# Kernel tuning notes

Measured on AMD Instinct MI355X. Metric: run time of the kernel, lower is better.

The kernel has to match this reference:

```python
import jax, jax.numpy as jnp
import numpy as np

N, L, E, H = 2, 2048, 1024, 16
DH = E // H  # head_dim = 64


def setup_inputs() -> dict:
    key = jax.random.key(0)
    ks = jax.random.split(key, 11)
    s_h = 1.0 / np.sqrt(DH)
    s_e = 1.0 / np.sqrt(E)
    return {
        "EP_q": jax.random.normal(ks[0], (N, L, E), jnp.float32),
        "EP_k": jax.random.normal(ks[1], (N, L, E), jnp.float32),
        "EP_v": jax.random.normal(ks[2], (N, L, E), jnp.float32),
        "W_q": jax.random.uniform(ks[3], (DH, DH), jnp.float32, -s_h, s_h),
        "b_q": jax.random.uniform(ks[4], (DH,), jnp.float32, -s_h, s_h),
        "W_k": jax.random.uniform(ks[5], (DH, DH), jnp.float32, -s_h, s_h),
        "b_k": jax.random.uniform(ks[6], (DH,), jnp.float32, -s_h, s_h),
        "W_v": jax.random.uniform(ks[7], (DH, DH), jnp.float32, -s_h, s_h),
        "b_v": jax.random.uniform(ks[8], (DH,), jnp.float32, -s_h, s_h),
        "W_o": jax.random.uniform(ks[9], (E, E), jnp.float32, -s_e, s_e),
        "b_o": jax.random.uniform(ks[10], (E,), jnp.float32, -s_e, s_e),
    }


def reference(EP_q, EP_k, EP_v, W_q, b_q, W_k, b_k, W_v, b_v, W_o, b_o):
    n, q_len = EP_q.shape[0], EP_q.shape[1]
    # split into heads: (N, L, H, DH)
    q = EP_q.reshape(n, q_len, H, DH)
    k = EP_k.reshape(n, EP_k.shape[1], H, DH)
    v = EP_v.reshape(n, EP_v.shape[1], H, DH)
    # per-head linear (same weights across heads), torch Linear: x @ W.T + b
    Q = q @ W_q.T + b_q
    K = k @ W_k.T + b_k
    V = v @ W_v.T + b_v
    # scores (N, H, Lq, Lk); NOTE: scaled by sqrt(embed_size) per original code
    scores = jnp.einsum("nqhd,nkhd->nhqk", Q, K) / jnp.sqrt(jnp.float32(E))
    attn = jax.nn.softmax(scores, axis=-1)
    out = jnp.einsum("nhqk,nkhd->nqhd", attn, V).reshape(n, q_len, E)
    return out @ W_o.T + b_o
```

## Files before the change

kernel.cpp:

```cpp
#include <hip/hip_runtime.h>

#define N_B 2
#define L_L 2048
#define E_E 1024
#define H_H 16
#define D_H 64
#define LDSP 72

typedef __bf16 bf16x8 __attribute__((ext_vector_type(8)));
typedef float f32x4 __attribute__((ext_vector_type(4)));
typedef short s16x8 __attribute__((ext_vector_type(8)));
typedef unsigned short u16x4 __attribute__((ext_vector_type(4)));

__device__ __forceinline__ f32x4 mfma16(bf16x8 a, bf16x8 b, f32x4 c) {
  return __builtin_amdgcn_mfma_f32_16x16x32_bf16(a, b, c, 0, 0, 0);
}

__device__ __forceinline__ unsigned short f2bf(float x) {
  unsigned int u = __float_as_uint(x);
  u = (u + 0x7fffu + ((u >> 16) & 1u)) >> 16;
  return (unsigned short)u;
}

__device__ __forceinline__ unsigned int cvtpk(float lo, float hi) {
  unsigned int r;
  asm("v_cvt_pk_bf16_f32 %0, %1, %2" : "=v"(r) : "v"(lo), "v"(hi));
  return r;
}

__device__ __forceinline__ void swap32(unsigned int& a, unsigned int& b) {
  asm("v_permlane32_swap_b32 %0, %1" : "+v"(a), "+v"(b));
}
__device__ __forceinline__ void swap16(unsigned int& a, unsigned int& b) {
  asm("v_permlane16_swap_b32 %0, %1" : "+v"(a), "+v"(b));
}

__device__ __forceinline__ float max3f(float a, float b, float c) {
  float r;
  asm("v_max3_f32 %0, %1, %2, %3" : "=v"(r) : "v"(a), "v"(b), "v"(c));
  return r;
}

__device__ __forceinline__ float exp2a(float x) {
  float r;
  asm("v_exp_f32 %0, %1" : "=v"(r) : "v"(x));
  return r;
}

__device__ __forceinline__ void gload16(const void* g, void* l) {
  __builtin_amdgcn_global_load_lds(
      (__attribute__((address_space(1))) void*)g,
      (__attribute__((address_space(3))) void*)l, 16, 0, 0);
}

__device__ __forceinline__ bf16x8 pack_frag(float p0, float p1, float p2, float p3,
                                            float p4, float p5, float p6, float p7) {
  unsigned int x0 = cvtpk(p0, p1), x1 = cvtpk(p2, p3);
  unsigned int x2 = cvtpk(p4, p5), x3 = cvtpk(p6, p7);
  swap32(x0, x2); swap16(x0, x2);
  swap32(x1, x3); swap16(x1, x3);
  union { unsigned int u[4]; bf16x8 v; } f;
  f.u[0] = x0; f.u[1] = x1; f.u[2] = x2; f.u[3] = x3;
  return f.v;
}

__global__ __launch_bounds__(256) void qkv_gemm_kernel(
    const float* __restrict__ EPq, const float* __restrict__ EPk, const float* __restrict__ EPv,
    const float* __restrict__ Wq, const float* __restrict__ Wk, const float* __restrict__ Wv,
    const float* __restrict__ bq, const float* __restrict__ bk, const float* __restrict__ bv,
    const float* __restrict__ Wo, unsigned short* __restrict__ Wob,
    unsigned short* __restrict__ Qb, unsigned short* __restrict__ Kb,
    unsigned short* __restrict__ Vtb) {
  __shared__ __attribute__((aligned(16))) unsigned short Xs[64][LDSP];
  __shared__ __attribute__((aligned(16))) unsigned short Ws[64][LDSP];
  const int tid = threadIdx.x;
  const int wid = tid >> 6;
  const int lane = tid & 63;
  const int lr = lane & 15;
  const int lg = lane >> 4;
  const int nh = blockIdx.x >> 5;
  const int l0 = (blockIdx.x & 31) * 64;
  const int n = nh >> 4;
  const int h = nh & 15;
  const float SCQ = 0.03125f * 1.44269504089f;

  {
    const int i = blockIdx.x * 256 + tid;
    const float4 f = ((const float4*)Wo)[i];
    u16x4 v = { f2bf(f.x), f2bf(f.y), f2bf(f.z), f2bf(f.w) };
    *(u16x4*)&Wob[(size_t)i * 4] = v;
  }

  #pragma unroll
  for (int mat = 0; mat < 3; ++mat) {
    const float* X = (mat == 0) ? EPq : (mat == 1) ? EPk : EPv;
    const float* W = (mat == 0) ? Wq : (mat == 1) ? Wk : Wv;
    const float* bias = (mat == 0) ? bq : (mat == 1) ? bk : bv;
    const float osc = (mat == 0) ? SCQ : 1.0f;

    const float* xb = X + ((size_t)(n * L_L + l0)) * E_E + h * D_H;
    #pragma unroll
    for (int it = 0; it < 4; ++it) {
      const int idx = it * 256 + tid;
      const int row = idx >> 4, c = idx & 15;
      const float4 f = *(const float4*)(xb + (size_t)row * E_E + c * 4);
      u16x4 v = { f2bf(f.x), f2bf(f.y), f2bf(f.z), f2bf(f.w) };
      *(u16x4*)&Xs[row][c * 4] = v;
    }
    #pragma unroll
    for (int it = 0; it < 4; ++it) {
      const int idx = it * 256 + tid;
      const int row = idx >> 4, c = idx & 15;
      const float4 f = *(const float4*)(W + idx * 4);
      u16x4 v = { f2bf(f.x), f2bf(f.y), f2bf(f.z), f2bf(f.w) };
      *(u16x4*)&Ws[row][c * 4] = v;
    }
    __syncthreads();

    const bf16x8 a0 = *(const bf16x8*)&Xs[wid * 16 + lr][lg * 8];
    const bf16x8 a1 = *(const bf16x8*)&Xs[wid * 16 + lr][32 + lg * 8];
    f32x4 acc[4];
    #pragma unroll
    for (int t = 0; t < 4; ++t) {
      const float bb = bias[t * 16 + lr];
      acc[t] = f32x4{bb, bb, bb, bb};
      const bf16x8 b0 = *(const bf16x8*)&Ws[t * 16 + lr][lg * 8];
      const bf16x8 b1 = *(const bf16x8*)&Ws[t * 16 + lr][32 + lg * 8];
      acc[t] = mfma16(a0, b0, acc[t]);
      acc[t] = mfma16(a1, b1, acc[t]);
    }
    __syncthreads();

    #pragma unroll
    for (int t = 0; t < 4; ++t)
      #pragma unroll
      for (int r = 0; r < 4; ++r)
        Xs[wid * 16 + lg * 4 + r][t * 16 + lr] = f2bf(acc[t][r] * osc);
    __syncthreads();

    if (mat < 2) {
      unsigned short* dst = ((mat == 0) ? Qb : Kb) + ((size_t)nh * L_L + l0) * D_H;
      #pragma unroll
      for (int it = 0; it < 2; ++it) {
        const int idx = it * 256 + tid;
        const int row = idx >> 3, c = idx & 7;
        *(s16x8*)(dst + (size_t)row * D_H + c * 8) = *(s16x8*)&Xs[row][c * 8];
      }
    } else {
      #pragma unroll
      for (int it = 0; it < 2; ++it) {
        const int idx = it * 256 + tid;
        const int d = idx & 63, c = idx >> 6;
        s16x8 v;
        #pragma unroll
        for (int j = 0; j < 8; ++j) v[j] = (short)Xs[c * 8 + j][d];
        *(s16x8*)(Vtb + ((size_t)nh * D_H + d) * L_L + l0 + c * 8) = v;
      }
    }
    __syncthreads();
  }
}

__global__ __launch_bounds__(512, 4) void attn_mfma_kernel(
    const unsigned short* __restrict__ Qb, const unsigned short* __restrict__ Kb,
    const unsigned short* __restrict__ Vtb, unsigned short* __restrict__ Ab) {
  __shared__ __attribute__((aligned(16))) unsigned short KS[2][2][64][64];
  __shared__ __attribute__((aligned(16))) unsigned short VS[2][2][64][64];

  const int tid = threadIdx.x;
  const int wid = tid >> 6;
  const int wq = wid & 3;
  const int kw = wid >> 2;
  const int lane = tid & 63;
  const int lr = lane & 15;
  const int lg = lane >> 4;

  const int bid = ((blockIdx.x & 7) << 6) + (blockIdx.x >> 3);
  const int nh = bid >> 4;
  const int q0w = ((bid & 15) << 7) + wq * 32;

  const unsigned short* gQ = Qb + ((size_t)nh * L_L + q0w) * D_H;

  bf16x8 bQ[2][2];
  #pragma unroll
  for (int qb = 0; qb < 2; ++qb)
    #pragma unroll
    for (int c2 = 0; c2 < 2; ++c2)
      bQ[qb][c2] = *(const bf16x8*)(gQ + (qb * 16 + lr) * D_H + c2 * 32 + lg * 8);

  const s16x8 ones16 = {0x3F80,0x3F80,0x3F80,0x3F80,0x3F80,0x3F80,0x3F80,0x3F80};
  const bf16x8 ones = *(const bf16x8*)&ones16;

  const int sh = tid >> 8;
  const int tid8 = tid & 255;
  const int srow0 = tid8 >> 3, sch0 = tid8 & 7;
  const int srow1 = srow0 + 32;
  const int kc0 = (sch0 ^ (srow0 & 7)) * 8;
  const int kc1 = (sch0 ^ (srow1 & 7)) * 8;
  const unsigned short* gKs = Kb + ((size_t)nh * L_L + sh * 1024) * D_H;
  const unsigned short* gVs = Vtb + (size_t)nh * D_H * L_L + sh * 1024;

  #define STAGE(buf, ktoff)                                                    \
    do {                                                                       \
      unsigned short* kd = &KS[sh][buf][0][0];                                 \
      unsigned short* vd = &VS[sh][buf][0][0];                                 \
      gload16(gKs + (size_t)((ktoff) * 64 + srow0) * D_H + kc0,                \
              kd + srow0 * 64 + sch0 * 8);                                     \
      gload16(gKs + (size_t)((ktoff) * 64 + srow1) * D_H + kc1,                \
              kd + srow1 * 64 + sch0 * 8);                                     \
      gload16(gVs + (size_t)srow0 * L_L + (ktoff) * 64 + kc0,                  \
              vd + srow0 * 64 + sch0 * 8);                                     \
      gload16(gVs + (size_t)srow1 * L_L + (ktoff) * 64 + kc1,                  \
              vd + srow1 * 64 + sch0 * 8);                                     \
    } while (0)

  STAGE(0, 0);
  __syncthreads();

  f32x4 acc0[4] = {f32x4{0,0,0,0},f32x4{0,0,0,0},f32x4{0,0,0,0},f32x4{0,0,0,0}};
  f32x4 acc1[4] = {f32x4{0,0,0,0},f32x4{0,0,0,0},f32x4{0,0,0,0},f32x4{0,0,0,0}};
  f32x4 lacc0 = {0,0,0,0}, lacc1 = {0,0,0,0};
  float m0 = -1e30f, m1 = -1e30f;
  int cur = 0;

  for (int kt = 0; kt < 16; ++kt) {
    STAGE(cur ^ 1, ((kt + 1) & 15));

    const char* Kcur = (const char*)&KS[kw][cur][0][0];
    const char* Vcur = (const char*)&VS[kw][cur][0][0];

    float sv0[16], sv1[16];
    __builtin_amdgcn_s_setprio(1);
    #pragma unroll
    for (int kb = 0; kb < 4; ++kb) {
      const int row = kb * 16 + lr;
      const bf16x8 a0 = *(const bf16x8*)(Kcur + row * 128 + ((lg ^ (row & 7)) << 4));
      const bf16x8 a1 = *(const bf16x8*)(Kcur + row * 128 + (((4 + lg) ^ (row & 7)) << 4));
      f32x4 c0 = {0,0,0,0}, c1 = {0,0,0,0};
      c0 = mfma16(a0, bQ[0][0], c0); c0 = mfma16(a1, bQ[0][1], c0);
      c1 = mfma16(a0, bQ[1][0], c1); c1 = mfma16(a1, bQ[1][1], c1);
      #pragma unroll
      for (int r = 0; r < 4; ++r) { sv0[kb*4+r] = c0[r]; sv1[kb*4+r] = c1[r]; }
    }
    __builtin_amdgcn_s_setprio(0);

    float mt0 = max3f(sv0[0], sv0[1], sv0[2]);
    float mt1 = max3f(sv1[0], sv1[1], sv1[2]);
    #pragma unroll
    for (int j = 3; j < 15; j += 2) {
      mt0 = max3f(mt0, sv0[j], sv0[j+1]);
      mt1 = max3f(mt1, sv1[j], sv1[j+1]);
    }
    mt0 = fmaxf(mt0, sv0[15]);
    mt1 = fmaxf(mt1, sv1[15]);

    const bool defer = (mt0 - m0 <= 8.0f) && (mt1 - m1 <= 8.0f);
    if (!__all(defer)) {
      float v0 = fmaxf(mt0, __shfl_xor(mt0, 16)); v0 = fmaxf(v0, __shfl_xor(v0, 32));
      float v1 = fmaxf(mt1, __shfl_xor(mt1, 16)); v1 = fmaxf(v1, __shfl_xor(v1, 32));
      const float mn0 = fmaxf(m0, v0), mn1 = fmaxf(m1, v1);
      const float sc0f = exp2a(m0 - mn0), sc1f = exp2a(m1 - mn1);
      m0 = mn0; m1 = mn1;
      #pragma unroll
      for (int r = 0; r < 4; ++r) {
        const float sa0 = __shfl(sc0f, 4 * lg + r);
        const float sa1 = __shfl(sc1f, 4 * lg + r);
        #pragma unroll
        for (int t = 0; t < 4; ++t) { acc0[t][r] *= sa0; acc1[t][r] *= sa1; }
        lacc0[r] *= sa0; lacc1[r] *= sa1;
      }
    }

    #pragma unroll
    for (int j = 0; j < 16; ++j) {
      sv0[j] = exp2a(sv0[j] - m0);
      sv1[j] = exp2a(sv1[j] - m1);
    }

    bf16x8 aP0[2], aP1[2];
    aP0[0] = pack_frag(sv0[0], sv0[1], sv0[2], sv0[3], sv0[4], sv0[5], sv0[6], sv0[7]);
    aP0[1] = pack_frag(sv0[8], sv0[9], sv0[10], sv0[11], sv0[12], sv0[13], sv0[14], sv0[15]);
    aP1[0] = pack_frag(sv1[0], sv1[1], sv1[2], sv1[3], sv1[4], sv1[5], sv1[6], sv1[7]);
    aP1[1] = pack_frag(sv1[8], sv1[9], sv1[10], sv1[11], sv1[12], sv1[13], sv1[14], sv1[15]);

    __builtin_amdgcn_s_setprio(1);
    lacc0 = mfma16(aP0[0], ones, lacc0); lacc0 = mfma16(aP0[1], ones, lacc0);
    lacc1 = mfma16(aP1[0], ones, lacc1); lacc1 = mfma16(aP1[1], ones, lacc1);
    #pragma unroll
    for (int t = 0; t < 4; ++t) {
      const int row = t * 16 + lr;
      const bf16x8 v0 = *(const bf16x8*)(Vcur + row * 128 + ((lg ^ (row & 7)) << 4));
      const bf16x8 v1 = *(const bf16x8*)(Vcur + row * 128 + (((4 + lg) ^ (row & 7)) << 4));
      acc0[t] = mfma16(aP0[0], v0, acc0[t]); acc0[t] = mfma16(aP0[1], v1, acc0[t]);
      acc1[t] = mfma16(aP1[0], v0, acc1[t]); acc1[t] = mfma16(aP1[1], v1, acc1[t]);
    }
    __builtin_amdgcn_s_setprio(0);

    __syncthreads();
    cur ^= 1;
  }
  #undef STAGE

  float mq0[4], mq1[4];
  #pragma unroll
  for (int r = 0; r < 4; ++r) {
    mq0[r] = __shfl(m0, 4 * lg + r);
    mq1[r] = __shfl(m1, 4 * lg + r);
  }
  float* accL = (float*)&KS[0][0][0][0];
  float* mlL  = (float*)&VS[0][0][0][0];
  if (kw == 1) {
    const int base = wq * 2048 + lane * 4;
    #pragma unroll
    for (int t = 0; t < 4; ++t) {
      *(f32x4*)&accL[base + t * 256] = acc0[t];
      *(f32x4*)&accL[base + 1024 + t * 256] = acc1[t];
    }
    if (lr == 0) {
      #pragma unroll
      for (int r = 0; r < 4; ++r) {
        const int q = 4 * lg + r;
        *(float2*)&mlL[wq * 128 + q * 2]      = float2{mq0[r], lacc0[r]};
        *(float2*)&mlL[wq * 128 + 64 + q * 2] = float2{mq1[r], lacc1[r]};
      }
    }
  }
  __syncthreads();
  if (kw == 0) {
    const int n = nh >> 4, h = nh & 15;
    const int base = wq * 2048 + lane * 4;
    #pragma unroll
    for (int qb = 0; qb < 2; ++qb) {
      const f32x4* accA = qb ? acc1 : acc0;
      const f32x4 lA4 = qb ? lacc1 : lacc0;
      const float* mqA = qb ? mq1 : mq0;
      #pragma unroll
      for (int r = 0; r < 4; ++r) {
        const int q = 4 * lg + r;
        const float2 mlB = *(const float2*)&mlL[wq * 128 + qb * 64 + q * 2];
        const float M = fmaxf(mqA[r], mlB.x);
        const float wA = exp2a(mqA[r] - M), wB = exp2a(mlB.x - M);
        const float invL = 1.0f / (lA4[r] * wA + mlB.y * wB);
        #pragma unroll
        for (int t = 0; t < 4; ++t) {
          const float ob = accL[base + qb * 1024 + t * 256 + r];
          const float o = (accA[t][r] * wA + ob * wB) * invL;
          Ab[((size_t)(n * L_L + q0w + qb * 16 + q)) * E_E + h * D_H + t * 16 + lr] =
              f2bf(o);
        }
      }
    }
  }
}

__global__ __launch_bounds__(256, 2) void out_gemm_kernel(
    const unsigned short* __restrict__ Ab, const unsigned short* __restrict__ Wob,
    const float* __restrict__ bo, float* __restrict__ out) {
  __shared__ __attribute__((aligned(16))) unsigned short As[2][64][64];
  __shared__ __attribute__((aligned(16))) unsigned short Bs[2][128][64];
  const int tid = threadIdx.x;
  const int wid = tid >> 6;
  const int lane = tid & 63;
  const int lr = lane & 15;
  const int lg = lane >> 4;

  const int bid = ((blockIdx.x & 7) << 6) + (blockIdx.x >> 3);
  const int m0 = (bid >> 3) * 64;
  const int n0 = (bid & 7) * 128;
  const int wr = wid >> 1, wc = wid & 1;

  const int r0 = tid >> 3, sc = tid & 7;
  const int scol = (sc ^ (r0 & 7)) * 8;

  #define OSTAGE(buf, kt)                                                      \
    do {                                                                       \
      unsigned short* ad = &As[buf][0][0];                                     \
      unsigned short* bd = &Bs[buf][0][0];                                     \
      gload16(Ab + (size_t)(m0 + r0) * E_E + (kt) * 64 + scol,                 \
              ad + r0 * 64 + sc * 8);                                          \
      gload16(Ab + (size_t)(m0 + r0 + 32) * E_E + (kt) * 64 + scol,            \
              ad + (r0 + 32) * 64 + sc * 8);                                   \
      gload16(Wob + (size_t)(n0 + r0) * E_E + (kt) * 64 + scol,                \
              bd + r0 * 64 + sc * 8);                                          \
      gload16(Wob + (size_t)(n0 + r0 + 32) * E_E + (kt) * 64 + scol,           \
              bd + (r0 + 32) * 64 + sc * 8);                                   \
      gload16(Wob + (size_t)(n0 + r0 + 64) * E_E + (kt) * 64 + scol,           \
              bd + (r0 + 64) * 64 + sc * 8);                                   \
      gload16(Wob + (size_t)(n0 + r0 + 96) * E_E + (kt) * 64 + scol,           \
              bd + (r0 + 96) * 64 + sc * 8);                                   \
    } while (0)

  f32x4 acc[2][4];
  #pragma unroll
  for (int mi = 0; mi < 2; ++mi)
    #pragma unroll
    for (int ni = 0; ni < 4; ++ni) {
      const float bb = bo[n0 + wc * 64 + ni * 16 + lr];
      acc[mi][ni] = f32x4{bb, bb, bb, bb};
    }

  OSTAGE(0, 0);
  __syncthreads();
  int cur = 0;

  for (int kt = 0; kt < 16; ++kt) {
    if (kt < 15) OSTAGE(cur ^ 1, kt + 1);

    const char* Ac = (const char*)&As[cur][0][0];
    const char* Bc = (const char*)&Bs[cur][0][0];
    bf16x8 af[2][2], bfr[4][2];
    #pragma unroll
    for (int mi = 0; mi < 2; ++mi) {
      const int row = wr * 32 + mi * 16 + lr;
      #pragma unroll
      for (int kb = 0; kb < 2; ++kb)
        af[mi][kb] = *(const bf16x8*)(Ac + row * 128 + (((kb * 4 + lg) ^ (row & 7)) << 4));
    }
    #pragma unroll
    for (int ni = 0; ni < 4; ++ni) {
      const int row = wc * 64 + ni * 16 + lr;
      #pragma unroll
      for (int kb = 0; kb < 2; ++kb)
        bfr[ni][kb] = *(const bf16x8*)(Bc + row * 128 + (((kb * 4 + lg) ^ (row & 7)) << 4));
    }
    __builtin_amdgcn_s_setprio(1);
    #pragma unroll
    for (int kb = 0; kb < 2; ++kb)
      #pragma unroll
      for (int mi = 0; mi < 2; ++mi)
        #pragma unroll
        for (int ni = 0; ni < 4; ++ni)
          acc[mi][ni] = mfma16(af[mi][kb], bfr[ni][kb], acc[mi][ni]);
    __builtin_amdgcn_s_setprio(0);

    __syncthreads();
    cur ^= 1;
  }
  #undef OSTAGE

  #pragma unroll
  for (int mi = 0; mi < 2; ++mi)
    #pragma unroll
    for (int ni = 0; ni < 4; ++ni) {
      const int nn = n0 + wc * 64 + ni * 16 + lr;
      #pragma unroll
      for (int r = 0; r < 4; ++r) {
        const int mm = m0 + wr * 32 + mi * 16 + lg * 4 + r;
        out[(size_t)mm * E_E + nn] = acc[mi][ni][r];
      }
    }
}

extern "C" void kernel_launch(void* const* d_in, const int* in_sizes, int n_in,
                              void* d_out, int out_size, void* d_ws, size_t ws_size,
                              hipStream_t stream) {
  const float* EPq = (const float*)d_in[0];
  const float* EPk = (const float*)d_in[1];
  const float* EPv = (const float*)d_in[2];
  const float* Wq  = (const float*)d_in[3];
  const float* bq  = (const float*)d_in[4];
  const float* Wk  = (const float*)d_in[5];
  const float* bk  = (const float*)d_in[6];
  const float* Wv  = (const float*)d_in[7];
  const float* bv  = (const float*)d_in[8];
  const float* Wo  = (const float*)d_in[9];
  const float* bo  = (const float*)d_in[10];
  float* out = (float*)d_out;

  unsigned short* ws = (unsigned short*)d_ws;
  const size_t SZ = (size_t)N_B * H_H * L_L * D_H;
  unsigned short* Qb  = ws;
  unsigned short* Kb  = Qb + SZ;
  unsigned short* Vtb = Kb + SZ;
  unsigned short* Ab  = Vtb + SZ;
  unsigned short* Wob = Ab + SZ;

  qkv_gemm_kernel<<<1024, 256, 0, stream>>>(
      EPq, EPk, EPv, Wq, Wk, Wv, bq, bk, bv, Wo, Wob, Qb, Kb, Vtb);
  attn_mfma_kernel<<<512, 512, 0, stream>>>(Qb, Kb, Vtb, Ab);
  out_gemm_kernel<<<512, 256, 0, stream>>>(Ab, Wob, bo, out);
}
```

Baseline: 79.69 us.

## Software-pipeline QK^T one tile ahead of softmax/PV with triple-buffered K

Restructures the attention main loop so the QK^T MFMAs for the next key tile are issued before the softmax and PV step of the current tile. K gets a three-slot LDS ring and V stays double-buffered, and the loop is unrolled by two with alternating score register sets. The aim is to overlap exp/max VALU work with matrix-core work and hide LDS latency. The cost is more LDS (one extra K slot) and roughly double the score registers, which may reduce occupancy under the 512x4 launch bound.

After: 219.4 us. +175.3%, slower.

```diff
diff --git a/kernel.cpp b/kernel.cpp
--- a/kernel.cpp
+++ b/kernel.cpp
@@ -164,7 +164,7 @@
 __global__ __launch_bounds__(512, 4) void attn_mfma_kernel(
     const unsigned short* __restrict__ Qb, const unsigned short* __restrict__ Kb,
     const unsigned short* __restrict__ Vtb, unsigned short* __restrict__ Ab) {
-  __shared__ __attribute__((aligned(16))) unsigned short KS[2][2][64][64];
+  __shared__ __attribute__((aligned(16))) unsigned short KS[3][2][64][64];
   __shared__ __attribute__((aligned(16))) unsigned short VS[2][2][64][64];
 
   const int tid = threadIdx.x;
@@ -200,106 +200,129 @@
   const unsigned short* gKs = Kb + ((size_t)nh * L_L + sh * 1024) * D_H;
   const unsigned short* gVs = Vtb + (size_t)nh * D_H * L_L + sh * 1024;
 
-  #define STAGE(buf, ktoff)                                                    \
+  #define STAGE_K(slot, ktt)                                                   \
     do {                                                                       \
-      unsigned short* kd = &KS[sh][buf][0][0];                                 \
-      unsigned short* vd = &VS[sh][buf][0][0];                                 \
-      gload16(gKs + (size_t)((ktoff) * 64 + srow0) * D_H + kc0,                \
+      unsigned short* kd = &KS[slot][sh][0][0];                                \
+      gload16(gKs + (size_t)((ktt) * 64 + srow0) * D_H + kc0,                  \
               kd + srow0 * 64 + sch0 * 8);                                     \
-      gload16(gKs + (size_t)((ktoff) * 64 + srow1) * D_H + kc1,                \
+      gload16(gKs + (size_t)((ktt) * 64 + srow1) * D_H + kc1,                  \
               kd + srow1 * 64 + sch0 * 8);                                     \
-      gload16(gVs + (size_t)srow0 * L_L + (ktoff) * 64 + kc0,                  \
+    } while (0)
+  #define STAGE_V(vb, ktt)                                                     \
+    do {                                                                       \
+      unsigned short* vd = &VS[vb][sh][0][0];                                  \
+      gload16(gVs + (size_t)srow0 * L_L + (ktt) * 64 + kc0,                    \
               vd + srow0 * 64 + sch0 * 8);                                     \
-      gload16(gVs + (size_t)srow1 * L_L + (ktoff) * 64 + kc1,                  \
+      gload16(gVs + (size_t)srow1 * L_L + (ktt) * 64 + kc1,                    \
               vd + srow1 * 64 + sch0 * 8);                                     \
     } while (0)
-
-  STAGE(0, 0);
-  __syncthreads();
 
   f32x4 acc0[4] = {f32x4{0,0,0,0},f32x4{0,0,0,0},f32x4{0,0,0,0},f32x4{0,0,0,0}};
   f32x4 acc1[4] = {f32x4{0,0,0,0},f32x4{0,0,0,0},f32x4{0,0,0,0},f32x4{0,0,0,0}};
   f32x4 lacc0 = {0,0,0,0}, lacc1 = {0,0,0,0};
   float m0 = -1e30f, m1 = -1e30f;
-  int cur = 0;
-
-  for (int kt = 0; kt < 16; ++kt) {
-    STAGE(cur ^ 1, ((kt + 1) & 15));
-
-    const char* Kcur = (const char*)&KS[kw][cur][0][0];
-    const char* Vcur = (const char*)&VS[kw][cur][0][0];
-
-    float sv0[16], sv1[16];
-    __builtin_amdgcn_s_setprio(1);
-    #pragma unroll
-    for (int kb = 0; kb < 4; ++kb) {
-      const int row = kb * 16 + lr;
-      const bf16x8 a0 = *(const bf16x8*)(Kcur + row * 128 + ((lg ^ (row & 7)) << 4));
-      const bf16x8 a1 = *(const bf16x8*)(Kcur + row * 128 + (((4 + lg) ^ (row & 7)) << 4));
-      f32x4 c0 = {0,0,0,0}, c1 = {0,0,0,0};
-      c0 = mfma16(a0, bQ[0][0], c0); c0 = mfma16(a1, bQ[0][1], c0);
-      c1 = mfma16(a0, bQ[1][0], c1); c1 = mfma16(a1, bQ[1][1], c1);
-      #pragma unroll
-      for (int r = 0; r < 4; ++r) { sv0[kb*4+r] = c0[r]; sv1[kb*4+r] = c1[r]; }
-    }
-    __builtin_amdgcn_s_setprio(0);
-
-    float mt0 = max3f(sv0[0], sv0[1], sv0[2]);
-    float mt1 = max3f(sv1[0], sv1[1], sv1[2]);
-    #pragma unroll
-    for (int j = 3; j < 15; j += 2) {
-      mt0 = max3f(mt0, sv0[j], sv0[j+1]);
-      mt1 = max3f(mt1, sv1[j], sv1[j+1]);
-    }
-    mt0 = fmaxf(mt0, sv0[15]);
-    mt1 = fmaxf(mt1, sv1[15]);
-
-    const bool defer = (mt0 - m0 <= 8.0f) && (mt1 - m1 <= 8.0f);
-    if (!__all(defer)) {
-      float v0 = fmaxf(mt0, __shfl_xor(mt0, 16)); v0 = fmaxf(v0, __shfl_xor(v0, 32));
-      float v1 = fmaxf(mt1, __shfl_xor(mt1, 16)); v1 = fmaxf(v1, __shfl_xor(v1, 32));
-      const float mn0 = fmaxf(m0, v0), mn1 = fmaxf(m1, v1);
-      const float sc0f = exp2a(m0 - mn0), sc1f = exp2a(m1 - mn1);
-      m0 = mn0; m1 = mn1;
-      #pragma unroll
-      for (int r = 0; r < 4; ++r) {
-        const float sa0 = __shfl(sc0f, 4 * lg + r);
-        const float sa1 = __shfl(sc1f, 4 * lg + r);
-        #pragma unroll
-        for (int t = 0; t < 4; ++t) { acc0[t][r] *= sa0; acc1[t][r] *= sa1; }
-        lacc0[r] *= sa0; lacc1[r] *= sa1;
+  float svA0[16], svA1[16], svB0[16], svB1[16];
+
+  #define QKT(SV0, SV1, ks)                                                    \
+    do {                                                                       \
+      const char* Kc = (const char*)&KS[ks][kw][0][0];                         \
+      _Pragma("unroll")                                                        \
+      for (int kb = 0; kb < 4; ++kb) {                                         \
+        const int row = kb * 16 + lr;                                          \
+        const bf16x8 a0 = *(const bf16x8*)(Kc + row * 128 + ((lg ^ (row & 7)) << 4)); \
+        const bf16x8 a1 = *(const bf16x8*)(Kc + row * 128 + (((4 + lg) ^ (row & 7)) << 4)); \
+        f32x4 c0 = {0,0,0,0}, c1 = {0,0,0,0};                                  \
+        c0 = mfma16(a0, bQ[0][0], c0); c0 = mfma16(a1, bQ[0][1], c0);          \
+        c1 = mfma16(a0, bQ[1][0], c1); c1 = mfma16(a1, bQ[1][1], c1);          \
+        _Pragma("unroll")                                                      \
+        for (int r = 0; r < 4; ++r) { SV0[kb*4+r] = c0[r]; SV1[kb*4+r] = c1[r]; } \
+      }                                                                        \
+    } while (0)
+
+  #define SMPV(SV0, SV1, vb)                                                   \
+    do {                                                                       \
+      float mt0 = max3f(SV0[0], SV0[1], SV0[2]);                               \
+      float mt1 = max3f(SV1[0], SV1[1], SV1[2]);                               \
+      _Pragma("unroll")                                                        \
+      for (int j = 3; j < 15; j += 2) {                                        \
+        mt0 = max3f(mt0, SV0[j], SV0[j+1]);                                    \
+        mt1 = max3f(mt1, SV1[j], SV1[j+1]);                                    \
+      }                                                                        \
+      mt0 = fmaxf(mt0, SV0[15]); mt1 = fmaxf(mt1, SV1[15]);                    \
+      const bool defer = (mt0 - m0 <= 8.0f) && (mt1 - m1 <= 8.0f);             \
+      if (!__all(defer)) {                                                     \
+        float v0 = fmaxf(mt0, __shfl_xor(mt0, 16)); v0 = fmaxf(v0, __shfl_xor(v0, 32)); \
+        float v1 = fmaxf(mt1, __shfl_xor(mt1, 16)); v1 = fmaxf(v1, __shfl_xor(v1, 32)); \
+        const float mn0 = fmaxf(m0, v0), mn1 = fmaxf(m1, v1);                  \
+        const float sc0f = exp2a(m0 - mn0), sc1f = exp2a(m1 - mn1);            \
+        m0 = mn0; m1 = mn1;                                                    \
+        _Pragma("unroll")                                                      \
+        for (int r = 0; r < 4; ++r) {                                          \
+          const float sa0 = __shfl(sc0f, 4 * lg + r);                          \
+          const float sa1 = __shfl(sc1f, 4 * lg + r);                          \
+          _Pragma("unroll")                                                    \
+          for (int t = 0; t < 4; ++t) { acc0[t][r] *= sa0; acc1[t][r] *= sa1; }\
+          lacc0[r] *= sa0; lacc1[r] *= sa1;                                    \
+        }                                                                      \
+      }                                                                        \
+      _Pragma("unroll")                                                        \
+      for (int j = 0; j < 16; ++j) {                                           \
+        SV0[j] = exp2a(SV0[j] - m0);                                           \
+        SV1[j] = exp2a(SV1[j] - m1);                                           \
+      }                                                                        \
+      bf16x8 aP0[2], aP1[2];                                                   \
+      aP0[0] = pack_frag(SV0[0], SV0[1], SV0[2], SV0[3], SV0[4], SV0[5], SV0[6], SV0[7]); \
+      aP0[1] = pack_frag(SV0[8], SV0[9], SV0[10], SV0[11], SV0[12], SV0[13], SV0[14], SV0[15]); \
+      aP1[0] = pack_frag(SV1[0], SV1[1], SV1[2], SV1[3], SV1[4], SV1[5], SV1[6], SV1[7]); \
+      aP1[1] = pack_frag(SV1[8], SV1[9], SV1[10], SV1[11], SV1[12], SV1[13], SV1[14], SV1[15]); \
+      const char* Vc = (const char*)&VS[vb][kw][0][0];                         \
+      __builtin_amdgcn_s_setprio(1);                                           \
+      lacc0 = mfma16(aP0[0], ones, lacc0); lacc0 = mfma16(aP0[1], ones, lacc0);\
+      lacc1 = mfma16(aP1[0], ones, lacc1); lacc1 = mfma16(aP1[1], ones, lacc1);\
+      _Pragma("unroll")                                                        \
+      for (int t = 0; t < 4; ++t) {                                            \
+        const int row = t * 16 + lr;                                           \
+        const bf16x8 v0 = *(const bf16x8*)(Vc + row * 128 + ((lg ^ (row & 7)) << 4)); \
+        const bf16x8 v1 = *(const bf16x8*)(Vc + row * 128 + (((4 + lg) ^ (row & 7)) << 4)); \
+        acc0[t] = mfma16(aP0[0], v0, acc0[t]); acc0[t] = mfma16(aP0[1], v1, acc0[t]); \
+        acc1[t] = mfma16(aP1[0], v0, acc1[t]); acc1[t] = mfma16(aP1[1], v1, acc1[t]); \
+      }                                                                        \
+      __builtin_amdgcn_s_setprio(0);                                           \
+    } while (0)
+
+  STAGE_K(0, 0);
+  STAGE_K(1, 1);
+  STAGE_V(0, 0);
+  __syncthreads();
+  QKT(svA0, svA1, 0);
+
+  int ksl_w = 2;
+  int ksl_r = 1;
+
+  for (int t2 = 0; t2 < 8; ++t2) {
+    {
+      const int t = 2 * t2;
+      if (t2 < 7) { STAGE_K(ksl_w, t + 2); ksl_w = (ksl_w == 2) ? 0 : ksl_w + 1; }
+      STAGE_V(1, t + 1);
+      QKT(svB0, svB1, ksl_r); ksl_r = (ksl_r == 2) ? 0 : ksl_r + 1;
+      SMPV(svA0, svA1, 0);
+      __syncthreads();
+    }
+    {
+      const int t = 2 * t2 + 1;
+      if (t2 < 7) {
+        STAGE_K(ksl_w, t + 2); ksl_w = (ksl_w == 2) ? 0 : ksl_w + 1;
+        STAGE_V(0, t + 1);
+        QKT(svA0, svA1, ksl_r); ksl_r = (ksl_r == 2) ? 0 : ksl_r + 1;
       }
-    }
-
-    #pragma unroll
-    for (int j = 0; j < 16; ++j) {
-      sv0[j] = exp2a(sv0[j] - m0);
-      sv1[j] = exp2a(sv1[j] - m1);
-    }
-
-    bf16x8 aP0[2], aP1[2];
-    aP0[0] = pack_frag(sv0[0], sv0[1], sv0[2], sv0[3], sv0[4], sv0[5], sv0[6], sv0[7]);
-    aP0[1] = pack_frag(sv0[8], sv0[9], sv0[10], sv0[11], sv0[12], sv0[13], sv0[14], sv0[15]);
-    aP1[0] = pack_frag(sv1[0], sv1[1], sv1[2], sv1[3], sv1[4], sv1[5], sv1[6], sv1[7]);
-    aP1[1] = pack_frag(sv1[8], sv1[9], sv1[10], sv1[11], sv1[12], sv1[13], sv1[14], sv1[15]);
-
-    __builtin_amdgcn_s_setprio(1);
-    lacc0 = mfma16(aP0[0], ones, lacc0); lacc0 = mfma16(aP0[1], ones, lacc0);
-    lacc1 = mfma16(aP1[0], ones, lacc1); lacc1 = mfma16(aP1[1], ones, lacc1);
-    #pragma unroll
-    for (int t = 0; t < 4; ++t) {
-      const int row = t * 16 + lr;
-      const bf16x8 v0 = *(const bf16x8*)(Vcur + row * 128 + ((lg ^ (row & 7)) << 4));
-      const bf16x8 v1 = *(const bf16x8*)(Vcur + row * 128 + (((4 + lg) ^ (row & 7)) << 4));
-      acc0[t] = mfma16(aP0[0], v0, acc0[t]); acc0[t] = mfma16(aP0[1], v1, acc0[t]);
-      acc1[t] = mfma16(aP1[0], v0, acc1[t]); acc1[t] = mfma16(aP1[1], v1, acc1[t]);
-    }
-    __builtin_amdgcn_s_setprio(0);
-
-    __syncthreads();
-    cur ^= 1;
-  }
-  #undef STAGE
+      SMPV(svB0, svB1, 1);
+      __syncthreads();
+    }
+  }
+  #undef STAGE_K
+  #undef STAGE_V
+  #undef QKT
+  #undef SMPV
 
   float mq0[4], mq1[4];
   #pragma unroll
```
